# Kernel optimization log

Hardware: AMD Instinct MI355X
Metric: run time of the kernel (lower is better)

## Reference

```python
import jax, jax.numpy as jnp
import numpy as np

R = 5          # number of rating values (relations)
U = 100000     # num users (user_in_units, one-hot ids)
M = 50000      # num items (movie_in_units)
E = 2000000    # edges per rating etype
F = 10         # internal feature dim (hardcoded in module)
D = 50         # per-relation msg dim = msg_units // R = 250 // 5


def setup_inputs() -> dict:
    key = jax.random.key(0)
    ks = jax.random.split(key, 12)
    f = lambda k, shape: jax.random.normal(k, shape, dtype=jnp.float32) * 0.1
    return {
        "edges_src": jax.random.randint(ks[0], (R, E), 0, U, dtype=jnp.int32),  # user endpoint
        "edges_dst": jax.random.randint(ks[1], (R, E), 0, M, dtype=jnp.int32),  # item endpoint
        # per-rating learned node-feature tables (feat1/feat2 of each GCMCGraphSage)
        "feat_u_fwd": f(ks[2], (R, U, F)),  # src feats for user->item conv
        "feat_i_fwd": f(ks[3], (R, M, F)),  # dst feats for user->item conv
        "feat_i_rev": f(ks[4], (R, M, F)),  # src feats for item->user (rev) conv
        "feat_u_rev": f(ks[5], (R, U, F)),  # dst feats for item->user (rev) conv
        # SAGEConv weights per relation (fc_self, fc_neigh, bias)
        "w_self_fwd": f(ks[6], (R, F, D)),
        "w_neigh_fwd": f(ks[7], (R, F, D)),
        "b_fwd": jnp.zeros((R, D), jnp.float32),
        "w_self_rev": f(ks[8], (R, F, D)),
        "w_neigh_rev": f(ks[9], (R, F, D)),
        "b_rev": jnp.zeros((R, D), jnp.float32),
    }


def _sage(feat_src, feat_dst, src, dst, w_self, w_neigh, b, n_dst):
    """DGL SAGEConv 'mean' on a bipartite relation: h = fc_self(x_dst) + fc_neigh(mean_j x_src[j]) + b."""
    msg = feat_src[src]                                               # (E, F) irregular gather
    s = jax.ops.segment_sum(msg, dst, num_segments=n_dst)             # (n_dst, F) scatter-add
    cnt = jax.ops.segment_sum(jnp.ones_like(dst, dtype=feat_src.dtype), dst, num_segments=n_dst)
    h_neigh = s / jnp.maximum(cnt, 1.0)[:, None]                      # zero in-degree -> 0 (DGL mean)
    return feat_dst @ w_self + h_neigh @ w_neigh + b


def reference(edges_src, edges_dst, feat_u_fwd, feat_i_fwd, feat_i_rev, feat_u_rev,
              w_self_fwd, w_neigh_fwd, b_fwd, w_self_rev, w_neigh_rev, b_rev):
    # rating etype: user -> item
    item_per = jax.vmap(lambda fs, fd, s, d, ws, wn, b: _sage(fs, fd, s, d, ws, wn, b, M))(
        feat_u_fwd, feat_i_fwd, edges_src, edges_dst, w_self_fwd, w_neigh_fwd, b_fwd)  # (R, M, D)
    # rev-rating etype: item -> user (edge direction reversed)
    user_per = jax.vmap(lambda fs, fd, s, d, ws, wn, b: _sage(fs, fd, s, d, ws, wn, b, U))(
        feat_i_rev, feat_u_rev, edges_dst, edges_src, w_self_rev, w_neigh_rev, b_rev)  # (R, U, D)
    # HeteroGraphConv aggregate='stack' -> (N, R, D); layer then flattens to (N, R*D)
    ufeat = jnp.transpose(user_per, (1, 0, 2)).reshape(U, R * D)
    ifeat = jnp.transpose(item_per, (1, 0, 2)).reshape(M, R * D)
    return (ufeat, ifeat)
```

## Files before the change

kernel.cpp:

```cpp
#include <hip/hip_runtime.h>

#define R 5
#define U 100000
#define M 50000
#define E 2000000
#define F 10
#define D 50

#define TE (R * E)
#define NBLK 192
#define CHUNK ((TE + NBLK - 1) / NBLK)
#define BSZ 256

#define NKEY_U 128
#define NKEY_I 64
#define KS_U (R * U)
#define KS_I (R * M)
#define NBU_U ((KS_U + NKEY_U - 1) / NKEY_U)
#define NBU_I ((KS_I + NKEY_I - 1) / NKEY_I)
#define NBU_T (NBU_U + NBU_I)
#define OFFI (NBU_U * NBLK)
#define GTOT (OFFI + NBU_I * NBLK)
#define NS1 ((GTOT + 1023) / 1024)
#define S2K ((NS1 + 255) / 256)

#define CAP 3328
#define ASTR 11


__global__ __launch_bounds__(BSZ) void phaseA(const int* __restrict__ esrc,
                                              const int* __restrict__ edst,
                                              unsigned* __restrict__ ghist) {
    __shared__ unsigned hist[NBU_T];
    for (int i = threadIdx.x; i < NBU_T; i += BSZ) hist[i] = 0;
    __syncthreads();
    int b = blockIdx.x;
    int lo = b * CHUNK, hi = min(lo + CHUNK, TE);
    for (int i = lo + threadIdx.x; i < hi; i += BSZ) {
        unsigned r = (unsigned)i / (unsigned)E;
        int s = esrc[i], d = edst[i];
        unsigned ku = r * U + (unsigned)s;
        unsigned ki = r * M + (unsigned)d;
        atomicAdd(&hist[ku >> 7], 1u);
        atomicAdd(&hist[NBU_U + (ki >> 6)], 1u);
    }
    __syncthreads();
    for (int j = threadIdx.x; j < NBU_T; j += BSZ) {
        unsigned idx = (j < NBU_U) ? (unsigned)j * NBLK + b
                                   : OFFI + (unsigned)(j - NBU_U) * NBLK + b;
        ghist[idx] = hist[j];
    }
}

__global__ __launch_bounds__(BSZ) void scan1(unsigned* __restrict__ S,
                                             unsigned* __restrict__ psum) {
    __shared__ unsigned sh[BSZ];
    int base = blockIdx.x * 1024 + threadIdx.x * 4;
    unsigned v[4], tsum = 0;
    for (int k = 0; k < 4; k++) {
        int i = base + k;
        v[k] = (i < GTOT) ? S[i] : 0u;
        tsum += v[k];
    }
    sh[threadIdx.x] = tsum;
    __syncthreads();
    for (int off = 1; off < BSZ; off <<= 1) {
        unsigned t = (threadIdx.x >= off) ? sh[threadIdx.x - off] : 0u;
        __syncthreads();
        sh[threadIdx.x] += t;
        __syncthreads();
    }
    unsigned ex = sh[threadIdx.x] - tsum;
    for (int k = 0; k < 4; k++) {
        int i = base + k;
        if (i < GTOT) S[i] = ex;
        ex += v[k];
    }
    if (threadIdx.x == BSZ - 1) psum[blockIdx.x] = sh[BSZ - 1];
}

__global__ __launch_bounds__(BSZ) void scan2(unsigned* __restrict__ psum) {
    __shared__ unsigned sh[BSZ];
    unsigned v[S2K], tsum = 0;
    int base = threadIdx.x * S2K;
    for (int k = 0; k < S2K; k++) {
        int i = base + k;
        v[k] = (i < NS1) ? psum[i] : 0u;
        tsum += v[k];
    }
    sh[threadIdx.x] = tsum;
    __syncthreads();
    for (int off = 1; off < BSZ; off <<= 1) {
        unsigned t = (threadIdx.x >= off) ? sh[threadIdx.x - off] : 0u;
        __syncthreads();
        sh[threadIdx.x] += t;
        __syncthreads();
    }
    unsigned ex = sh[threadIdx.x] - tsum;
    for (int k = 0; k < S2K; k++) {
        int i = base + k;
        if (i < NS1) psum[i] = ex;
        ex += v[k];
    }
}

__global__ __launch_bounds__(BSZ) void scan3(unsigned* __restrict__ S,
                                             const unsigned* __restrict__ psum) {
    unsigned add = psum[blockIdx.x];
    int base = blockIdx.x * 1024 + threadIdx.x * 4;
    for (int k = 0; k < 4; k++) {
        int i = base + k;
        if (i < GTOT) S[i] += add;
    }
}

__global__ __launch_bounds__(BSZ) void phaseC(const int* __restrict__ esrc,
                                              const int* __restrict__ edst,
                                              const unsigned* __restrict__ S,
                                              unsigned* __restrict__ sorted) {
    __shared__ unsigned cur[NBU_T];
    int b = blockIdx.x;
    for (int j = threadIdx.x; j < NBU_T; j += BSZ) {
        unsigned idx = (j < NBU_U) ? (unsigned)j * NBLK + b
                                   : OFFI + (unsigned)(j - NBU_U) * NBLK + b;
        cur[j] = S[idx];
    }
    __syncthreads();
    int lo = b * CHUNK, hi = min(lo + CHUNK, TE);
    for (int i = lo + threadIdx.x; i < hi; i += BSZ) {
        unsigned r = (unsigned)i / (unsigned)E;
        int s = esrc[i], d = edst[i];
        unsigned ku = r * U + (unsigned)s;
        unsigned ki = r * M + (unsigned)d;
        unsigned pu = atomicAdd(&cur[ku >> 7], 1u);
        sorted[pu] = (ku & 127u) | ((unsigned)d << 7);
        unsigned pi = atomicAdd(&cur[NBU_U + (ki >> 6)], 1u);
        sorted[pi] = (ki & 63u) | ((unsigned)s << 6);
    }
}

__global__ __launch_bounds__(BSZ, 8) void phaseD(
    const unsigned* __restrict__ sorted, const unsigned* __restrict__ S,
    const float* __restrict__ fsrc_u, const float* __restrict__ fdst_u,
    const float* __restrict__ wsf_u, const float* __restrict__ wnf_u,
    const float* __restrict__ bia_u,
    const float* __restrict__ fsrc_i, const float* __restrict__ fdst_i,
    const float* __restrict__ wsf_i, const float* __restrict__ wnf_i,
    const float* __restrict__ bia_i,
    float* __restrict__ out_u, float* __restrict__ out_i) {
    __shared__ unsigned sbuf[CAP];
    __shared__ float acc[NKEY_U * ASTR];
    __shared__ unsigned hist[NKEY_U];
    __shared__ unsigned cur[NKEY_U];
    __shared__ unsigned rbase[NKEY_U];

    unsigned orig = blockIdx.x;
    unsigned bkt;
    {
        unsigned o = (orig < NBU_U) ? orig : orig - NBU_U;
        const unsigned q = NBU_U / 8u, rem = NBU_U % 8u;
        unsigned x = o & 7u, off = o >> 3;
        unsigned m = (x < rem ? x * (q + 1u) : rem * (q + 1u) + (x - rem) * q) + off;
        bkt = (orig < NBU_U) ? m : NBU_U + m;
    }

    bool isU = bkt < NBU_U;
    int j = isU ? (int)bkt : (int)bkt - NBU_U;
    unsigned N = isU ? U : M;
    unsigned NSRC = isU ? M : U;
    unsigned NKEY = isU ? NKEY_U : NKEY_I;
    unsigned KM = NKEY - 1u;
    unsigned KSH = isU ? 7u : 6u;
    const float* fsrc = isU ? fsrc_u : fsrc_i;

    unsigned sbase = isU ? 0u : (unsigned)OFFI;
    unsigned lo = S[sbase + (unsigned)j * NBLK];
    unsigned hi = (!isU && j + 1 == NBU_I) ? (unsigned)(2 * TE)
                                           : S[sbase + (unsigned)(j + 1) * NBLK];
    unsigned len = hi - lo;
    unsigned keybase = (unsigned)j * NKEY;
    int tid = threadIdx.x;

    for (int t = tid; t < NKEY_U * ASTR; t += BSZ) acc[t] = 0.f;
    if (tid < NKEY_U) {
        hist[tid] = 0u;
        unsigned key = keybase + (unsigned)tid;
        unsigned r = (key < (unsigned)R * N) ? key / N : 0u;
        rbase[tid] = r * NSRC;
    }
    __syncthreads();

    if (len <= CAP) {
        for (unsigned e = lo + tid; e < hi; e += BSZ)
            atomicAdd(&hist[sorted[e] & KM], 1u);
        __syncthreads();
        if (tid < NKEY_U) cur[tid] = hist[tid];
        __syncthreads();
        for (int off = 1; off < NKEY_U; off <<= 1) {
            unsigned t = 0;
            if (tid < NKEY_U && tid >= off) t = cur[tid - off];
            __syncthreads();
            if (tid < NKEY_U && tid >= off) cur[tid] += t;
            __syncthreads();
        }
        if (tid < NKEY_U) cur[tid] -= hist[tid];
        __syncthreads();
        for (unsigned e = lo + tid; e < hi; e += BSZ) {
            unsigned pay = sorted[e];
            unsigned pos = atomicAdd(&cur[pay & KM], 1u);
            sbuf[pos] = pay;
        }
        __syncthreads();
        unsigned L = (len + BSZ - 1) / BSZ;
        unsigned i0 = (unsigned)tid * L;
        unsigned i1 = min(i0 + L, len);
        if (i0 < i1) {
            int curKey = -1;
            float A0 = 0, A1 = 0, A2 = 0, A3 = 0, A4 = 0,
                  A5 = 0, A6 = 0, A7 = 0, A8 = 0, A9 = 0;
#define FLUSH_ACC()                                                        \
    do {                                                                   \
        if (curKey >= 0) {                                                 \
            float* ap = acc + curKey * ASTR;                               \
            atomicAdd(ap + 0, A0); atomicAdd(ap + 1, A1);                  \
            atomicAdd(ap + 2, A2); atomicAdd(ap + 3, A3);                  \
            atomicAdd(ap + 4, A4); atomicAdd(ap + 5, A5);                  \
            atomicAdd(ap + 6, A6); atomicAdd(ap + 7, A7);                  \
            atomicAdd(ap + 8, A8); atomicAdd(ap + 9, A9);                  \
        }                                                                  \
    } while (0)
#define ZERO_ACC() A0=A1=A2=A3=A4=A5=A6=A7=A8=A9=0.f
            unsigned i = i0;
            for (; i + 1 < i1; i += 2) {
                unsigned p0 = sbuf[i], p1 = sbuf[i + 1];
                unsigned k0 = p0 & KM, s0 = p0 >> KSH;
                unsigned k1 = p1 & KM, s1 = p1 >> KSH;
                const float2* r0 = (const float2*)(fsrc + (size_t)(rbase[k0] + s0) * F);
                const float2* r1 = (const float2*)(fsrc + (size_t)(rbase[k1] + s1) * F);
                float2 x0 = r0[0], x1 = r0[1], x2 = r0[2], x3 = r0[3], x4 = r0[4];
                float2 y0 = r1[0], y1 = r1[1], y2 = r1[2], y3 = r1[3], y4 = r1[4];
                if ((int)k0 != curKey) { FLUSH_ACC(); curKey = (int)k0; ZERO_ACC(); }
                A0 += x0.x; A1 += x0.y; A2 += x1.x; A3 += x1.y; A4 += x2.x;
                A5 += x2.y; A6 += x3.x; A7 += x3.y; A8 += x4.x; A9 += x4.y;
                if ((int)k1 != curKey) { FLUSH_ACC(); curKey = (int)k1; ZERO_ACC(); }
                A0 += y0.x; A1 += y0.y; A2 += y1.x; A3 += y1.y; A4 += y2.x;
                A5 += y2.y; A6 += y3.x; A7 += y3.y; A8 += y4.x; A9 += y4.y;
            }
            if (i < i1) {
                unsigned p0 = sbuf[i];
                unsigned k0 = p0 & KM, s0 = p0 >> KSH;
                const float2* r0 = (const float2*)(fsrc + (size_t)(rbase[k0] + s0) * F);
                float2 x0 = r0[0], x1 = r0[1], x2 = r0[2], x3 = r0[3], x4 = r0[4];
                if ((int)k0 != curKey) { FLUSH_ACC(); curKey = (int)k0; ZERO_ACC(); }
                A0 += x0.x; A1 += x0.y; A2 += x1.x; A3 += x1.y; A4 += x2.x;
                A5 += x2.y; A6 += x3.x; A7 += x3.y; A8 += x4.x; A9 += x4.y;
            }
            FLUSH_ACC();
#undef FLUSH_ACC
#undef ZERO_ACC
        }
    } else {
        for (unsigned e = lo + tid; e < hi; e += BSZ) {
            unsigned pay = sorted[e];
            unsigned l = pay & KM, s = pay >> KSH;
            const float2* row = (const float2*)(fsrc + (size_t)(rbase[l] + s) * F);
            float* a = acc + l * ASTR;
#pragma unroll
            for (int k = 0; k < 5; k++) {
                float2 v = row[k];
                atomicAdd(a + 2 * k, v.x);
                atomicAdd(a + 2 * k + 1, v.y);
            }
            atomicAdd(&hist[l], 1u);
        }
    }
    __syncthreads();

    const float* fdst = isU ? fdst_u : fdst_i;
    const float* wsf = isU ? wsf_u : wsf_i;
    const float* wnf = isU ? wnf_u : wnf_i;
    const float* bia = isU ? bia_u : bia_i;
    float* out = isU ? out_u : out_i;

    int tot = (int)NKEY * D;
    for (int o = tid; o < tot; o += BSZ) {
        int local = o / D, d = o - local * D;
        unsigned key = keybase + (unsigned)local;
        if (key >= (unsigned)(R)*N) continue;
        unsigned r = key / N, n = key - r * N;
        float inv = 1.f / fmaxf((float)hist[local], 1.f);
        const float* fd = fdst + ((size_t)r * N + n) * F;
        const float* a = acc + local * ASTR;
        const float* wsp = wsf + (size_t)r * F * D + d;
        const float* wnp = wnf + (size_t)r * F * D + d;
        float o1 = bia[r * D + d], o2 = 0.f;
#pragma unroll
        for (int f = 0; f < F; f++) {
            o1 += fd[f] * wsp[(size_t)f * D];
            o2 += a[f] * wnp[(size_t)f * D];
        }
        out[(size_t)n * (R * D) + r * D + d] = o1 + o2 * inv;
    }
}

#define SUM_I_OFF 0
#define CNT_I_OFF ((size_t)R * M * F)
#define SUM_U_OFF (CNT_I_OFF + (size_t)R * M)
#define CNT_U_OFF (SUM_U_OFF + (size_t)R * U * F)
#define WS_FLOATS (CNT_U_OFF + (size_t)R * U)

__global__ void scatter_edges(const int* __restrict__ esrc, const int* __restrict__ edst,
                              const float* __restrict__ feat_u_fwd,
                              const float* __restrict__ feat_i_rev, float* __restrict__ ws) {
    float* sum_i = ws + SUM_I_OFF;
    float* cnt_i = ws + CNT_I_OFF;
    float* sum_u = ws + SUM_U_OFF;
    float* cnt_u = ws + CNT_U_OFF;
    const int total = R * E;
    for (int idx = blockIdx.x * blockDim.x + threadIdx.x; idx < total;
         idx += gridDim.x * blockDim.x) {
        int r = idx / E;
        int s = esrc[idx], d = edst[idx];
        const float* fu = feat_u_fwd + ((size_t)r * U + s) * F;
        const float* fi = feat_i_rev + ((size_t)r * M + d) * F;
        float* si = sum_i + ((size_t)r * M + d) * F;
        float* su = sum_u + ((size_t)r * U + s) * F;
#pragma unroll
        for (int f = 0; f < F; ++f) {
            atomicAdd(si + f, fu[f]);
            atomicAdd(su + f, fi[f]);
        }
        atomicAdd(cnt_i + (size_t)r * M + d, 1.0f);
        atomicAdd(cnt_u + (size_t)r * U + s, 1.0f);
    }
}

__global__ void finalize_nodes(int N, const float* __restrict__ feat_dst,
                               const float* __restrict__ w_self, const float* __restrict__ w_neigh,
                               const float* __restrict__ bias, const float* __restrict__ sum,
                               const float* __restrict__ cnt, float* __restrict__ out) {
    int idx = blockIdx.x * blockDim.x + threadIdx.x;
    int total = N * R * D;
    if (idx >= total) return;
    int n = idx / (R * D);
    int rd = idx - n * (R * D);
    int r = rd / D;
    int d = rd - r * D;
    const float* fd = feat_dst + ((size_t)r * N + n) * F;
    const float* sn = sum + ((size_t)r * N + n) * F;
    float inv = 1.0f / fmaxf(cnt[(size_t)r * N + n], 1.0f);
    const float* wsp = w_self + (size_t)r * F * D + d;
    const float* wnp = w_neigh + (size_t)r * F * D + d;
    float acc_self = bias[r * D + d];
    float acc_n = 0.0f;
#pragma unroll
    for (int f = 0; f < F; ++f) {
        acc_self += fd[f] * wsp[(size_t)f * D];
        acc_n += sn[f] * wnp[(size_t)f * D];
    }
    out[idx] = acc_self + acc_n * inv;
}

extern "C" void kernel_launch(void* const* d_in, const int* in_sizes, int n_in,
                              void* d_out, int out_size, void* d_ws, size_t ws_size,
                              hipStream_t stream) {
    const int* edges_src = (const int*)d_in[0];
    const int* edges_dst = (const int*)d_in[1];
    const float* feat_u_fwd = (const float*)d_in[2];
    const float* feat_i_fwd = (const float*)d_in[3];
    const float* feat_i_rev = (const float*)d_in[4];
    const float* feat_u_rev = (const float*)d_in[5];
    const float* w_self_fwd = (const float*)d_in[6];
    const float* w_neigh_fwd = (const float*)d_in[7];
    const float* b_fwd = (const float*)d_in[8];
    const float* w_self_rev = (const float*)d_in[9];
    const float* w_neigh_rev = (const float*)d_in[10];
    const float* b_rev = (const float*)d_in[11];

    float* out = (float*)d_out;
    float* out_u = out;
    float* out_i = out + (size_t)U * R * D;

    size_t need = ((size_t)2 * TE + (size_t)GTOT + 2048ull) * 4ull;
    if (ws_size >= need) {
        unsigned* sorted = (unsigned*)d_ws;
        unsigned* S = sorted + (size_t)2 * TE;
        unsigned* psum = S + GTOT;

        phaseA<<<NBLK, BSZ, 0, stream>>>(edges_src, edges_dst, S);
        scan1<<<NS1, BSZ, 0, stream>>>(S, psum);
        scan2<<<1, BSZ, 0, stream>>>(psum);
        scan3<<<NS1, BSZ, 0, stream>>>(S, psum);
        phaseC<<<NBLK, BSZ, 0, stream>>>(edges_src, edges_dst, S, sorted);
        phaseD<<<NBU_T, BSZ, 0, stream>>>(sorted, S,
                                          feat_i_rev, feat_u_rev, w_self_rev, w_neigh_rev, b_rev,
                                          feat_u_fwd, feat_i_fwd, w_self_fwd, w_neigh_fwd, b_fwd,
                                          out_u, out_i);
    } else {
        float* ws = (float*)d_ws;
        hipMemsetAsync(d_ws, 0, WS_FLOATS * sizeof(float), stream);
        scatter_edges<<<4096, 256, 0, stream>>>(edges_src, edges_dst, feat_u_fwd, feat_i_rev, ws);
        finalize_nodes<<<(U * R * D + 255) / 256, 256, 0, stream>>>(
            U, feat_u_rev, w_self_rev, w_neigh_rev, b_rev, ws + SUM_U_OFF, ws + CNT_U_OFF, out_u);
        finalize_nodes<<<(M * R * D + 255) / 256, 256, 0, stream>>>(
            M, feat_i_fwd, w_self_fwd, w_neigh_fwd, b_fwd, ws + SUM_I_OFF, ws + CNT_I_OFF, out_i);
    }
}
```

Measured before the change: 742.6 us.

## Split user/item bucket sorts into separate passes and gather bf16-packed feature rows

Source feature tables are pre-converted to bf16 and packed into 32-byte rows, so each edge gather reads one aligned 16B load plus one word instead of five float2 loads. The combined two-direction counting sort becomes two templated passes, one per direction, which reuse the sorted buffer and have fewer buckets each. The partitioning block count rises from 192 to 1024. This trades extra kernel launches, two conversion passes and bf16 rounding error in the neighbour sums for less gather traffic and smaller shared histograms.

```diff
diff --git a/kernel.cpp b/kernel.cpp
--- a/kernel.cpp
+++ b/kernel.cpp
@@ -8,48 +8,57 @@
 #define D 50
 
 #define TE (R * E)
-#define NBLK 192
+#define NBLK 1024
 #define CHUNK ((TE + NBLK - 1) / NBLK)
 #define BSZ 256
 
-#define NKEY_U 128
-#define NKEY_I 64
-#define KS_U (R * U)
-#define KS_I (R * M)
-#define NBU_U ((KS_U + NKEY_U - 1) / NKEY_U)
-#define NBU_I ((KS_I + NKEY_I - 1) / NKEY_I)
-#define NBU_T (NBU_U + NBU_I)
-#define OFFI (NBU_U * NBLK)
-#define GTOT (OFFI + NBU_I * NBLK)
-#define NS1 ((GTOT + 1023) / 1024)
+#define NKEY0 128
+#define NKEY1 64
+#define NBU 3907
+#define GT2 (NBU * NBLK)
+#define NS1 ((GT2 + 1023) / 1024)
 #define S2K ((NS1 + 255) / 256)
 
 #define CAP 3328
 #define ASTR 11
 
-
-__global__ __launch_bounds__(BSZ) void phaseA(const int* __restrict__ esrc,
-                                              const int* __restrict__ edst,
+__global__ __launch_bounds__(BSZ) void prep_bf16(const float* __restrict__ src,
+                                                 unsigned* __restrict__ dst,
+                                                 int nrows) {
+    int row = blockIdx.x * blockDim.x + threadIdx.x;
+    if (row >= nrows) return;
+    const float2* s2 = (const float2*)(src + (size_t)row * F);
+    unsigned w[5];
+#pragma unroll
+    for (int k = 0; k < 5; k++) {
+        float2 v = s2[k];
+        unsigned lo = __float_as_uint(v.x);
+        unsigned hi = __float_as_uint(v.y);
+        lo = (lo + 0x7FFFu + ((lo >> 16) & 1u)) >> 16;
+        hi = (hi + 0x7FFFu + ((hi >> 16) & 1u)) & 0xFFFF0000u;
+        w[k] = lo | hi;
+    }
+    uint4* d = (uint4*)(dst + (size_t)row * 8);
+    d[0] = make_uint4(w[0], w[1], w[2], w[3]);
+    d[1] = make_uint4(w[4], 0u, 0u, 0u);
+}
+
+template<int NN, int KSH>
+__global__ __launch_bounds__(BSZ) void phaseA(const int* __restrict__ keys,
                                               unsigned* __restrict__ ghist) {
-    __shared__ unsigned hist[NBU_T];
-    for (int i = threadIdx.x; i < NBU_T; i += BSZ) hist[i] = 0;
+    __shared__ unsigned hist[NBU];
+    for (int i = threadIdx.x; i < NBU; i += BSZ) hist[i] = 0;
     __syncthreads();
     int b = blockIdx.x;
     int lo = b * CHUNK, hi = min(lo + CHUNK, TE);
     for (int i = lo + threadIdx.x; i < hi; i += BSZ) {
         unsigned r = (unsigned)i / (unsigned)E;
-        int s = esrc[i], d = edst[i];
-        unsigned ku = r * U + (unsigned)s;
-        unsigned ki = r * M + (unsigned)d;
-        atomicAdd(&hist[ku >> 7], 1u);
-        atomicAdd(&hist[NBU_U + (ki >> 6)], 1u);
-    }
-    __syncthreads();
-    for (int j = threadIdx.x; j < NBU_T; j += BSZ) {
-        unsigned idx = (j < NBU_U) ? (unsigned)j * NBLK + b
-                                   : OFFI + (unsigned)(j - NBU_U) * NBLK + b;
-        ghist[idx] = hist[j];
-    }
+        unsigned key = r * (unsigned)NN + (unsigned)keys[i];
+        atomicAdd(&hist[key >> KSH], 1u);
+    }
+    __syncthreads();
+    for (int j = threadIdx.x; j < NBU; j += BSZ)
+        ghist[(size_t)j * NBLK + b] = hist[j];
 }
 
 __global__ __launch_bounds__(BSZ) void scan1(unsigned* __restrict__ S,
@@ -59,7 +68,7 @@
     unsigned v[4], tsum = 0;
     for (int k = 0; k < 4; k++) {
         int i = base + k;
-        v[k] = (i < GTOT) ? S[i] : 0u;
+        v[k] = (i < GT2) ? S[i] : 0u;
         tsum += v[k];
     }
     sh[threadIdx.x] = tsum;
@@ -73,7 +82,7 @@
     unsigned ex = sh[threadIdx.x] - tsum;
     for (int k = 0; k < 4; k++) {
         int i = base + k;
-        if (i < GTOT) S[i] = ex;
+        if (i < GT2) S[i] = ex;
         ex += v[k];
     }
     if (threadIdx.x == BSZ - 1) psum[blockIdx.x] = sh[BSZ - 1];
@@ -110,83 +119,77 @@
     int base = blockIdx.x * 1024 + threadIdx.x * 4;
     for (int k = 0; k < 4; k++) {
         int i = base + k;
-        if (i < GTOT) S[i] += add;
-    }
-}
-
-__global__ __launch_bounds__(BSZ) void phaseC(const int* __restrict__ esrc,
-                                              const int* __restrict__ edst,
+        if (i < GT2) S[i] += add;
+    }
+}
+
+template<int NN, int KSH>
+__global__ __launch_bounds__(BSZ) void phaseC(const int* __restrict__ keys,
+                                              const int* __restrict__ other,
                                               const unsigned* __restrict__ S,
                                               unsigned* __restrict__ sorted) {
-    __shared__ unsigned cur[NBU_T];
+    __shared__ unsigned cur[NBU];
     int b = blockIdx.x;
-    for (int j = threadIdx.x; j < NBU_T; j += BSZ) {
-        unsigned idx = (j < NBU_U) ? (unsigned)j * NBLK + b
-                                   : OFFI + (unsigned)(j - NBU_U) * NBLK + b;
-        cur[j] = S[idx];
-    }
+    for (int j = threadIdx.x; j < NBU; j += BSZ)
+        cur[j] = S[(size_t)j * NBLK + b];
     __syncthreads();
     int lo = b * CHUNK, hi = min(lo + CHUNK, TE);
+    const unsigned KM = (1u << KSH) - 1u;
     for (int i = lo + threadIdx.x; i < hi; i += BSZ) {
         unsigned r = (unsigned)i / (unsigned)E;
-        int s = esrc[i], d = edst[i];
-        unsigned ku = r * U + (unsigned)s;
-        unsigned ki = r * M + (unsigned)d;
-        unsigned pu = atomicAdd(&cur[ku >> 7], 1u);
-        sorted[pu] = (ku & 127u) | ((unsigned)d << 7);
-        unsigned pi = atomicAdd(&cur[NBU_U + (ki >> 6)], 1u);
-        sorted[pi] = (ki & 63u) | ((unsigned)s << 6);
-    }
-}
-
+        unsigned key = r * (unsigned)NN + (unsigned)keys[i];
+        unsigned pos = atomicAdd(&cur[key >> KSH], 1u);
+        sorted[pos] = (key & KM) | ((unsigned)other[i] << KSH);
+    }
+}
+
+__device__ __forceinline__ unsigned bucket_swizzle(unsigned o) {
+    const unsigned q = NBU / 8u, rem = NBU % 8u;
+    unsigned x = o & 7u, off = o >> 3;
+    return (x < rem ? x * (q + 1u) : rem * (q + 1u) + (x - rem) * q) + off;
+}
+
+#define ADDROW(A, B)                                                        \
+    do {                                                                    \
+        A0 += __uint_as_float((A).x << 16);                                 \
+        A1 += __uint_as_float((A).x & 0xFFFF0000u);                         \
+        A2 += __uint_as_float((A).y << 16);                                 \
+        A3 += __uint_as_float((A).y & 0xFFFF0000u);                         \
+        A4 += __uint_as_float((A).z << 16);                                 \
+        A5 += __uint_as_float((A).z & 0xFFFF0000u);                         \
+        A6 += __uint_as_float((A).w << 16);                                 \
+        A7 += __uint_as_float((A).w & 0xFFFF0000u);                         \
+        A8 += __uint_as_float((B) << 16);                                   \
+        A9 += __uint_as_float((B) & 0xFFFF0000u);                           \
+    } while (0)
+
+template<int N, int NSRC, int NKEY, int KSH>
 __global__ __launch_bounds__(BSZ, 8) void phaseD(
     const unsigned* __restrict__ sorted, const unsigned* __restrict__ S,
-    const float* __restrict__ fsrc_u, const float* __restrict__ fdst_u,
-    const float* __restrict__ wsf_u, const float* __restrict__ wnf_u,
-    const float* __restrict__ bia_u,
-    const float* __restrict__ fsrc_i, const float* __restrict__ fdst_i,
-    const float* __restrict__ wsf_i, const float* __restrict__ wnf_i,
-    const float* __restrict__ bia_i,
-    float* __restrict__ out_u, float* __restrict__ out_i) {
+    const unsigned* __restrict__ bsrc,
+    const float* __restrict__ fdst, const float* __restrict__ wsf,
+    const float* __restrict__ wnf, const float* __restrict__ bia,
+    float* __restrict__ out) {
     __shared__ unsigned sbuf[CAP];
-    __shared__ float acc[NKEY_U * ASTR];
-    __shared__ unsigned hist[NKEY_U];
-    __shared__ unsigned cur[NKEY_U];
-    __shared__ unsigned rbase[NKEY_U];
-
-    unsigned orig = blockIdx.x;
-    unsigned bkt;
-    {
-        unsigned o = (orig < NBU_U) ? orig : orig - NBU_U;
-        const unsigned q = NBU_U / 8u, rem = NBU_U % 8u;
-        unsigned x = o & 7u, off = o >> 3;
-        unsigned m = (x < rem ? x * (q + 1u) : rem * (q + 1u) + (x - rem) * q) + off;
-        bkt = (orig < NBU_U) ? m : NBU_U + m;
-    }
-
-    bool isU = bkt < NBU_U;
-    int j = isU ? (int)bkt : (int)bkt - NBU_U;
-    unsigned N = isU ? U : M;
-    unsigned NSRC = isU ? M : U;
-    unsigned NKEY = isU ? NKEY_U : NKEY_I;
-    unsigned KM = NKEY - 1u;
-    unsigned KSH = isU ? 7u : 6u;
-    const float* fsrc = isU ? fsrc_u : fsrc_i;
-
-    unsigned sbase = isU ? 0u : (unsigned)OFFI;
-    unsigned lo = S[sbase + (unsigned)j * NBLK];
-    unsigned hi = (!isU && j + 1 == NBU_I) ? (unsigned)(2 * TE)
-                                           : S[sbase + (unsigned)(j + 1) * NBLK];
+    __shared__ float acc[NKEY0 * ASTR];
+    __shared__ unsigned hist[NKEY0];
+    __shared__ unsigned cur[NKEY0];
+    __shared__ unsigned rbase[NKEY0];
+
+    unsigned j = bucket_swizzle(blockIdx.x);
+    const unsigned KM = (unsigned)NKEY - 1u;
+    unsigned lo = S[(size_t)j * NBLK];
+    unsigned hi = (j + 1 == NBU) ? (unsigned)TE : S[(size_t)(j + 1) * NBLK];
     unsigned len = hi - lo;
-    unsigned keybase = (unsigned)j * NKEY;
+    unsigned keybase = j * (unsigned)NKEY;
     int tid = threadIdx.x;
 
-    for (int t = tid; t < NKEY_U * ASTR; t += BSZ) acc[t] = 0.f;
-    if (tid < NKEY_U) {
+    for (int t = tid; t < NKEY * ASTR; t += BSZ) acc[t] = 0.f;
+    if (tid < NKEY) {
         hist[tid] = 0u;
         unsigned key = keybase + (unsigned)tid;
-        unsigned r = (key < (unsigned)R * N) ? key / N : 0u;
-        rbase[tid] = r * NSRC;
+        unsigned r = (key < (unsigned)R * N) ? key / (unsigned)N : 0u;
+        rbase[tid] = r * (unsigned)NSRC;
     }
     __syncthreads();
 
@@ -194,16 +197,16 @@
         for (unsigned e = lo + tid; e < hi; e += BSZ)
             atomicAdd(&hist[sorted[e] & KM], 1u);
         __syncthreads();
-        if (tid < NKEY_U) cur[tid] = hist[tid];
-        __syncthreads();
-        for (int off = 1; off < NKEY_U; off <<= 1) {
+        if (tid < NKEY) cur[tid] = hist[tid];
+        __syncthreads();
+        for (int off = 1; off < NKEY; off <<= 1) {
             unsigned t = 0;
-            if (tid < NKEY_U && tid >= off) t = cur[tid - off];
+            if (tid < NKEY && tid >= off) t = cur[tid - off];
             __syncthreads();
-            if (tid < NKEY_U && tid >= off) cur[tid] += t;
+            if (tid < NKEY && tid >= off) cur[tid] += t;
             __syncthreads();
         }
-        if (tid < NKEY_U) cur[tid] -= hist[tid];
+        if (tid < NKEY) cur[tid] -= hist[tid];
         __syncthreads();
         for (unsigned e = lo + tid; e < hi; e += BSZ) {
             unsigned pay = sorted[e];
@@ -235,25 +238,25 @@
                 unsigned p0 = sbuf[i], p1 = sbuf[i + 1];
                 unsigned k0 = p0 & KM, s0 = p0 >> KSH;
                 unsigned k1 = p1 & KM, s1 = p1 >> KSH;
-                const float2* r0 = (const float2*)(fsrc + (size_t)(rbase[k0] + s0) * F);
-                const float2* r1 = (const float2*)(fsrc + (size_t)(rbase[k1] + s1) * F);
-                float2 x0 = r0[0], x1 = r0[1], x2 = r0[2], x3 = r0[3], x4 = r0[4];
-                float2 y0 = r1[0], y1 = r1[1], y2 = r1[2], y3 = r1[3], y4 = r1[4];
+                const unsigned* r0 = bsrc + (size_t)(rbase[k0] + s0) * 8;
+                const unsigned* r1 = bsrc + (size_t)(rbase[k1] + s1) * 8;
+                uint4 xa = *(const uint4*)r0;
+                unsigned xb = r0[4];
+                uint4 ya = *(const uint4*)r1;
+                unsigned yb = r1[4];
                 if ((int)k0 != curKey) { FLUSH_ACC(); curKey = (int)k0; ZERO_ACC(); }
-                A0 += x0.x; A1 += x0.y; A2 += x1.x; A3 += x1.y; A4 += x2.x;
-                A5 += x2.y; A6 += x3.x; A7 += x3.y; A8 += x4.x; A9 += x4.y;
+                ADDROW(xa, xb);
                 if ((int)k1 != curKey) { FLUSH_ACC(); curKey = (int)k1; ZERO_ACC(); }
-                A0 += y0.x; A1 += y0.y; A2 += y1.x; A3 += y1.y; A4 += y2.x;
-                A5 += y2.y; A6 += y3.x; A7 += y3.y; A8 += y4.x; A9 += y4.y;
+                ADDROW(ya, yb);
             }
             if (i < i1) {
                 unsigned p0 = sbuf[i];
                 unsigned k0 = p0 & KM, s0 = p0 >> KSH;
-                const float2* r0 = (const float2*)(fsrc + (size_t)(rbase[k0] + s0) * F);
-                float2 x0 = r0[0], x1 = r0[1], x2 = r0[2], x3 = r0[3], x4 = r0[4];
+                const unsigned* r0 = bsrc + (size_t)(rbase[k0] + s0) * 8;
+                uint4 xa = *(const uint4*)r0;
+                unsigned xb = r0[4];
                 if ((int)k0 != curKey) { FLUSH_ACC(); curKey = (int)k0; ZERO_ACC(); }
-                A0 += x0.x; A1 += x0.y; A2 += x1.x; A3 += x1.y; A4 += x2.x;
-                A5 += x2.y; A6 += x3.x; A7 += x3.y; A8 += x4.x; A9 += x4.y;
+                ADDROW(xa, xb);
             }
             FLUSH_ACC();
 #undef FLUSH_ACC
@@ -263,31 +266,31 @@
         for (unsigned e = lo + tid; e < hi; e += BSZ) {
             unsigned pay = sorted[e];
             unsigned l = pay & KM, s = pay >> KSH;
-            const float2* row = (const float2*)(fsrc + (size_t)(rbase[l] + s) * F);
-            float* a = acc + l * ASTR;
-#pragma unroll
-            for (int k = 0; k < 5; k++) {
-                float2 v = row[k];
-                atomicAdd(a + 2 * k, v.x);
-                atomicAdd(a + 2 * k + 1, v.y);
-            }
+            const unsigned* rp = bsrc + (size_t)(rbase[l] + s) * 8;
+            uint4 a = *(const uint4*)rp;
+            unsigned b = rp[4];
+            float* ap = acc + l * ASTR;
+            atomicAdd(ap + 0, __uint_as_float(a.x << 16));
+            atomicAdd(ap + 1, __uint_as_float(a.x & 0xFFFF0000u));
+            atomicAdd(ap + 2, __uint_as_float(a.y << 16));
+            atomicAdd(ap + 3, __uint_as_float(a.y & 0xFFFF0000u));
+            atomicAdd(ap + 4, __uint_as_float(a.z << 16));
+            atomicAdd(ap + 5, __uint_as_float(a.z & 0xFFFF0000u));
+            atomicAdd(ap + 6, __uint_as_float(a.w << 16));
+            atomicAdd(ap + 7, __uint_as_float(a.w & 0xFFFF0000u));
+            atomicAdd(ap + 8, __uint_as_float(b << 16));
+            atomicAdd(ap + 9, __uint_as_float(b & 0xFFFF0000u));
             atomicAdd(&hist[l], 1u);
         }
     }
     __syncthreads();
 
-    const float* fdst = isU ? fdst_u : fdst_i;
-    const float* wsf = isU ? wsf_u : wsf_i;
-    const float* wnf = isU ? wnf_u : wnf_i;
-    const float* bia = isU ? bia_u : bia_i;
-    float* out = isU ? out_u : out_i;
-
-    int tot = (int)NKEY * D;
+    int tot = NKEY * D;
     for (int o = tid; o < tot; o += BSZ) {
         int local = o / D, d = o - local * D;
         unsigned key = keybase + (unsigned)local;
-        if (key >= (unsigned)(R)*N) continue;
-        unsigned r = key / N, n = key - r * N;
+        if (key >= (unsigned)R * N) continue;
+        unsigned r = key / (unsigned)N, n = key - r * (unsigned)N;
         float inv = 1.f / fmaxf((float)hist[local], 1.f);
         const float* fd = fdst + ((size_t)r * N + n) * F;
         const float* a = acc + local * ASTR;
@@ -381,21 +384,37 @@
     float* out_u = out;
     float* out_i = out + (size_t)U * R * D;
 
-    size_t need = ((size_t)2 * TE + (size_t)GTOT + 2048ull) * 4ull;
-    if (ws_size >= need) {
-        unsigned* sorted = (unsigned*)d_ws;
-        unsigned* S = sorted + (size_t)2 * TE;
-        unsigned* psum = S + GTOT;
-
-        phaseA<<<NBLK, BSZ, 0, stream>>>(edges_src, edges_dst, S);
+    size_t o_S = (size_t)TE;
+    size_t o_psum = o_S + GT2;
+    size_t o_bfu = o_psum + 4096;
+    size_t o_bfi = o_bfu + (size_t)R * U * 8;
+    size_t tot_u32 = o_bfi + (size_t)R * M * 8;
+    if (ws_size >= tot_u32 * 4ull) {
+        unsigned* ws32 = (unsigned*)d_ws;
+        unsigned* sorted = ws32;
+        unsigned* S = ws32 + o_S;
+        unsigned* psum = ws32 + o_psum;
+        unsigned* bfu = ws32 + o_bfu;
+        unsigned* bfi = ws32 + o_bfi;
+
+        prep_bf16<<<(R * U + BSZ - 1) / BSZ, BSZ, 0, stream>>>(feat_u_fwd, bfu, R * U);
+        prep_bf16<<<(R * M + BSZ - 1) / BSZ, BSZ, 0, stream>>>(feat_i_rev, bfi, R * M);
+
+        phaseA<U, 7><<<NBLK, BSZ, 0, stream>>>(edges_src, S);
         scan1<<<NS1, BSZ, 0, stream>>>(S, psum);
         scan2<<<1, BSZ, 0, stream>>>(psum);
         scan3<<<NS1, BSZ, 0, stream>>>(S, psum);
-        phaseC<<<NBLK, BSZ, 0, stream>>>(edges_src, edges_dst, S, sorted);
-        phaseD<<<NBU_T, BSZ, 0, stream>>>(sorted, S,
-                                          feat_i_rev, feat_u_rev, w_self_rev, w_neigh_rev, b_rev,
-                                          feat_u_fwd, feat_i_fwd, w_self_fwd, w_neigh_fwd, b_fwd,
-                                          out_u, out_i);
+        phaseC<U, 7><<<NBLK, BSZ, 0, stream>>>(edges_src, edges_dst, S, sorted);
+        phaseD<U, M, NKEY0, 7><<<NBU, BSZ, 0, stream>>>(
+            sorted, S, bfi, feat_u_rev, w_self_rev, w_neigh_rev, b_rev, out_u);
+
+        phaseA<M, 6><<<NBLK, BSZ, 0, stream>>>(edges_dst, S);
+        scan1<<<NS1, BSZ, 0, stream>>>(S, psum);
+        scan2<<<1, BSZ, 0, stream>>>(psum);
+        scan3<<<NS1, BSZ, 0, stream>>>(S, psum);
+        phaseC<M, 6><<<NBLK, BSZ, 0, stream>>>(edges_dst, edges_src, S, sorted);
+        phaseD<M, U, NKEY1, 6><<<NBU, BSZ, 0, stream>>>(
+            sorted, S, bfu, feat_i_fwd, w_self_fwd, w_neigh_fwd, b_fwd, out_i);
     } else {
         float* ws = (float*)d_ws;
         hipMemsetAsync(d_ws, 0, WS_FLOATS * sizeof(float), stream);
```

Result: slower. 955.8 us (+28.7%).
